# Optimization experiments

Hardware: AMD Instinct MI355X
Metric: run time of the kernel (lower is better)

Reference implementation:

```python
import jax, jax.numpy as jnp
import numpy as np

S = 32   # parent grid side
G = 64   # child grid side (2*S)
C = 16   # channels
DN = ('NDHWC', 'DHWIO', 'NDHWC')


def conv3(t, w, b):
    # t: [D,H,W,Cin] dense grid; zero padding == nonexistent coords contribute 0 (ME semantics)
    return jax.lax.conv_general_dilated(t[None], w, (1, 1, 1), 'SAME', dimension_numbers=DN)[0] + b


def _grids():
    ix = jnp.arange(G)
    px = (ix % 2)[:, None, None]
    py = (ix % 2)[None, :, None]
    pz = (ix % 2)[None, None, :]
    oct_m = {(a, b, c): (px == a) & (py == b) & (pz == c)
             for a in (0, 1) for b in (0, 1) for c in (0, 1)}
    groups6 = [[(0, 0, 0)], [(1, 1, 0)], [(1, 0, 1)], [(0, 1, 1)],
               [(1, 0, 0), (0, 1, 0)], [(0, 0, 1), (1, 1, 1)]]
    g6 = [jnp.any(jnp.stack([oct_m[o] for o in g]), 0) for g in groups6]
    s3 = (ix // 2)[:, None, None] + (ix // 2)[None, :, None] + (ix // 2)[None, None, :]
    m3 = [(s3 % 3) == j for j in range(3)]  # 3-way repartition (group_mask_gen_par)
    return g6, m3


def coder(feat, occ, w1, b1, w2, b2):
    # ProbCoder: conv -> ReLU -> conv -> sigmoid; outputs exist only at input coords
    of = occ[..., None].astype(feat.dtype)
    h = jax.nn.relu(conv3(feat, w1, b1)) * of
    return jax.nn.sigmoid(conv3(h, w2, b2)) * of


def union(a, b):
    (fa, oa), (fb, ob) = a, b
    return (jnp.where(oa[..., None], fa, fb), oa | ob)


def _forward(x, w_down, b_down, w_fel1, b_fel1, w_fel2, b_fel2, w_up, b_up,
             wc1, bc1, wc2, bc2, wl1, bl1, wl2, bl2):
    g6, m3 = _grids()
    occ_x = x[..., 0] > 0                                    # GT occupied child voxels
    # down (stride-2 conv): coordinate effect only -- last_POV uses ones_like features
    p_occ = jnp.any(occ_x.reshape(S, 2, S, 2, S, 2), axis=(1, 3, 5))  # parent coords
    pf = p_occ[..., None].astype(x.dtype)                    # last_POV features (ones)
    # FEL (dfa): conv(1->C,k3)+ReLU+conv(C->C,k3), outputs only at existing parents
    h = jax.nn.relu(conv3(pf, w_fel1, b_fel1)) * pf
    h = conv3(h, w_fel2, b_fel2) * pf                        # [S,S,S,C]
    # generative transposed conv k2 s2: each parent emits 8 children (octant-specific weight)
    up = jnp.einsum('xyzc,ocd->xyzod', h, w_up) + b_up       # [S,S,S,8,C]
    up = up.reshape(S, S, S, 2, 2, 2, C).transpose(0, 3, 1, 4, 2, 5, 6).reshape(G, G, G, C)
    occ = jnp.repeat(jnp.repeat(jnp.repeat(p_occ, 2, 0), 2, 1), 2, 2)  # child coords of prob
    prob_f = up * occ[..., None]
    lab = [occ_x & g for g in g6]                            # generate_label: GT per group
    # ---------- anchor1 compression (3 sub-stages inside octant group 1) ----------
    a1_o = occ & g6[0]
    a1_f = prob_f * a1_o[..., None]
    r = [(a1_f * m[..., None], a1_o & m) for m in m3]
    lab1 = [lab[0] & m for m in m3]
    p11 = coder(r[0][0], r[0][1], wc1[0], bc1[0], wc2[0], bc2[0])
    d1s = (prob_f * lab1[0][..., None], lab1[0])             # decoded GT of sub-stage 1
    in2 = union(r[1], d1s)
    p12 = coder(in2[0], in2[1], wl1[0], bl1[0], wl2[0], bl2[0]) * (in2[1] & m3[1])[..., None]
    d2s = (prob_f * lab1[1][..., None], lab1[1])
    in3 = union(union(d1s, d2s), r[2])
    p13 = coder(in3[0], in3[1], wl1[1], bl1[1], wl2[1], bl2[1]) * (in3[1] & m3[2])[..., None]
    # ---------- anchors 2..6 ----------
    dec = (prob_f * lab[0][..., None], lab[0])               # prob_anchor1_dec
    probs = [p11, p12, p13]
    for k in range(1, 6):
        ak_o = occ & g6[k]
        ak = (prob_f * ak_o[..., None], ak_o)
        inp = union(dec, ak)
        pk = coder(inp[0], inp[1], wc1[k], bc1[k], wc2[k], bc2[k]) * (inp[1] & g6[k])[..., None]
        probs.append(pk)
        if k < 5:
            dk = (prob_f * lab[k][..., None], lab[k])
            dec = union(dec, dk)
    probs = jnp.stack([p[..., 0] for p in probs], 0)          # [8,G,G,G]
    labels = jnp.stack([lab1[0], lab1[1], lab1[2], lab[1], lab[2], lab[3], lab[4], lab[5]], 0).astype(x.dtype)
    return probs, labels


def setup_inputs() -> dict:
    key = jax.random.key(0)
    ks = jax.random.split(key, 20)
    f = lambda k, s: jax.random.normal(k, s, jnp.float32) * 0.1
    x = (jax.random.uniform(ks[0], (G, G, G, 1)) < 0.5).astype(jnp.float32)
    return {
        'x': x,
        'w_down': f(ks[1], (2, 2, 2, 1, 1)), 'b_down': f(ks[2], (1,)),
        'w_fel1': f(ks[3], (3, 3, 3, 1, C)), 'b_fel1': f(ks[4], (C,)),
        'w_fel2': f(ks[5], (3, 3, 3, C, C)), 'b_fel2': f(ks[6], (C,)),
        'w_up': f(ks[7], (8, C, C)), 'b_up': f(ks[8], (C,)),
        'wc1': f(ks[9], (6, 3, 3, 3, C, C)), 'bc1': f(ks[10], (6, C)),
        'wc2': f(ks[11], (6, 3, 3, 3, C, 1)), 'bc2': f(ks[12], (6, 1)),
        'wl1': f(ks[13], (2, 5, 5, 5, C, C)), 'bl1': f(ks[14], (2, C)),
        'wl2': f(ks[15], (2, 5, 5, 5, C, 1)), 'bl2': f(ks[16], (2, 1)),
    }


def reference(x, w_down, b_down, w_fel1, b_fel1, w_fel2, b_fel2, w_up, b_up,
              wc1, bc1, wc2, bc2, wl1, bl1, wl2, bl2):
    return _forward(x, w_down, b_down, w_fel1, b_fel1, w_fel2, b_fel2, w_up, b_up,
                    wc1, bc1, wc2, bc2, wl1, bl1, wl2, bl2)
```

## Files before the change

kernel.cpp:

```cpp
#include <hip/hip_runtime.h>
#include <cstdint>
#include <math.h>

#define G 64
#define S 32
#define G3 (G*G*G)
#define S3 (S*S*S)

typedef unsigned long long u64;
typedef unsigned int u32;
typedef unsigned short u16;

typedef __attribute__((ext_vector_type(8))) short s16x8;
typedef __attribute__((ext_vector_type(4))) float f32x4;

__device__ __forceinline__ float sigmoidf_(float v) {
    return 1.0f / (1.0f + expf(-v));
}
__device__ __forceinline__ u32 f2bf_rne(float f) {
    u32 u = __float_as_uint(f);
    u += 0x7fff + ((u >> 16) & 1);
    return u >> 16;
}
__device__ __forceinline__ u64 rfl64(u64 v) {
    u32 lo = __builtin_amdgcn_readfirstlane((u32)v);
    u32 hi = __builtin_amdgcn_readfirstlane((u32)(v >> 32));
    return ((u64)hi << 32) | lo;
}
__device__ __forceinline__ u64 tap_hit(u64 wout, u64 wn, int dz) {
    return (dz >= 0) ? (wout & (wn >> dz)) : (wout & (wn << (-dz)));
}

__global__ __launch_bounds__(256) void k_pocc(const float* __restrict__ x,
                                              unsigned char* __restrict__ pocc) {
    int p = blockIdx.x * 256 + threadIdx.x;
    if (p >= S3) return;
    int pz = p & 31, py = (p >> 5) & 31, px = p >> 10;
    const float* b = x + (((size_t)(px * 2) * G + py * 2) * G + pz * 2);
    bool occ = false;
    #pragma unroll
    for (int a = 0; a < 2; a++)
        #pragma unroll
        for (int bb = 0; bb < 2; bb++)
            #pragma unroll
            for (int c = 0; c < 2; c++)
                occ = occ || (b[((size_t)a * G + bb) * G + c] > 0.0f);
    pocc[p] = occ ? 1 : 0;
}

__global__ __launch_bounds__(256) void k_fel1(const unsigned char* __restrict__ pocc,
                                              const float* __restrict__ w1,
                                              const float* __restrict__ b1,
                                              float* __restrict__ h1) {
    int p = blockIdx.x * 256 + threadIdx.x;
    if (p >= S3) return;
    int pz = p & 31, py = (p >> 5) & 31, px = p >> 10;
    float* o = h1 + (size_t)p * 16;
    if (!pocc[p]) {
        #pragma unroll
        for (int i = 0; i < 16; i++) o[i] = 0.0f;
        return;
    }
    float acc[16];
    #pragma unroll
    for (int i = 0; i < 16; i++) acc[i] = b1[i];
    for (int dx = -1; dx <= 1; ++dx) {
        int nx = px + dx; if ((unsigned)nx >= S) continue;
        for (int dy = -1; dy <= 1; ++dy) {
            int ny = py + dy; if ((unsigned)ny >= S) continue;
            for (int dz = -1; dz <= 1; ++dz) {
                int nz = pz + dz; if ((unsigned)nz >= S) continue;
                if (pocc[(nx * S + ny) * S + nz]) {
                    const float* w = w1 + (((dx + 1) * 3 + (dy + 1)) * 3 + (dz + 1)) * 16;
                    #pragma unroll
                    for (int i = 0; i < 16; i++) acc[i] += w[i];
                }
            }
        }
    }
    #pragma unroll
    for (int i = 0; i < 16; i++) o[i] = fmaxf(acc[i], 0.0f);
}

__global__ __launch_bounds__(256) void k_fel2(const unsigned char* __restrict__ pocc,
                                              const float* __restrict__ h1,
                                              const float* __restrict__ w2,
                                              const float* __restrict__ b2,
                                              float* __restrict__ h2) {
    int p = blockIdx.x * 256 + threadIdx.x;
    if (p >= S3) return;
    int pz = p & 31, py = (p >> 5) & 31, px = p >> 10;
    float* o = h2 + (size_t)p * 16;
    if (!pocc[p]) {
        #pragma unroll
        for (int i = 0; i < 16; i++) o[i] = 0.0f;
        return;
    }
    float acc[16];
    #pragma unroll
    for (int i = 0; i < 16; i++) acc[i] = b2[i];
    for (int dx = -1; dx <= 1; ++dx) {
        int nx = px + dx; if ((unsigned)nx >= S) continue;
        for (int dy = -1; dy <= 1; ++dy) {
            int ny = py + dy; if ((unsigned)ny >= S) continue;
            for (int dz = -1; dz <= 1; ++dz) {
                int nz = pz + dz; if ((unsigned)nz >= S) continue;
                const float* f = h1 + (size_t)((nx * S + ny) * S + nz) * 16;
                const float* w = w2 + (((dx + 1) * 3 + (dy + 1)) * 3 + (dz + 1)) * 256;
                #pragma unroll
                for (int ci = 0; ci < 16; ++ci) {
                    float fv = f[ci];
                    #pragma unroll
                    for (int co = 0; co < 16; ++co)
                        acc[co] = fmaf(fv, w[ci * 16 + co], acc[co]);
                }
            }
        }
    }
    #pragma unroll
    for (int i = 0; i < 16; i++) o[i] = acc[i];
}

__global__ __launch_bounds__(256) void k_up(const unsigned char* __restrict__ pocc,
                                            const float* __restrict__ h2,
                                            const float* __restrict__ wup,
                                            const float* __restrict__ bup,
                                            u16* __restrict__ pf) {
    int p = blockIdx.x * 256 + threadIdx.x;
    if (p >= S3) return;
    int pz = p & 31, py = (p >> 5) & 31, px = p >> 10;
    bool occ = pocc[p] != 0;
    float h[16];
    const float* hp = h2 + (size_t)p * 16;
    #pragma unroll
    for (int i = 0; i < 16; i++) h[i] = hp[i];
    #pragma unroll
    for (int o = 0; o < 8; o++) {
        int a = o >> 2, b = (o >> 1) & 1, c = o & 1;
        u16* op = pf + (((size_t)(2 * px + a) * G + (2 * py + b)) * G + (2 * pz + c)) * 16;
        uint4* o4 = reinterpret_cast<uint4*>(op);
        if (!occ) {
            o4[0] = make_uint4(0, 0, 0, 0);
            o4[1] = make_uint4(0, 0, 0, 0);
        } else {
            u32 pk[8];
            #pragma unroll
            for (int i = 0; i < 8; ++i) {
                float a0 = bup[2 * i], a1 = bup[2 * i + 1];
                #pragma unroll
                for (int cc = 0; cc < 16; cc++) {
                    a0 = fmaf(h[cc], wup[(o * 16 + cc) * 16 + 2 * i], a0);
                    a1 = fmaf(h[cc], wup[(o * 16 + cc) * 16 + 2 * i + 1], a1);
                }
                pk[i] = f2bf_rne(a0) | (f2bf_rne(a1) << 16);
            }
            o4[0] = make_uint4(pk[0], pk[1], pk[2], pk[3]);
            o4[1] = make_uint4(pk[4], pk[5], pk[6], pk[7]);
        }
    }
}

__global__ __launch_bounds__(256) void k_masks(const float* __restrict__ x,
                                               const unsigned char* __restrict__ pocc,
                                               u64* __restrict__ lw_in,
                                               u64* __restrict__ lw_fin,
                                               float* __restrict__ labels) {
    int z = threadIdx.x;
    int y = blockIdx.x * 4 + threadIdx.y;
    int xx = blockIdx.y;
    int v = (xx * G + y) * G + z;
    int par = ((xx & 1) << 2) | ((y & 1) << 1) | (z & 1);
    const int gmap[8] = {0, 5, 4, 3, 4, 2, 1, 5};
    int g = gmap[par];
    int t = ((xx >> 1) + (y >> 1) + (z >> 1)) % 3;
    bool occ = pocc[(((xx >> 1) * S) + (y >> 1)) * S + (z >> 1)] != 0;
    bool ox = x[v] > 0.0f;
    bool g0 = (g == 0);

    bool mi[8], mf[8], lb[8];
    mi[0] = occ && g0 && (t == 0);
    mi[1] = (occ && g0 && (t == 1)) || (ox && g0 && (t == 0));
    mi[2] = (ox && g0 && (t < 2)) || (occ && g0 && (t == 2));
    mi[3] = (ox && g0)       || (occ && (g == 1));
    mi[4] = (ox && (g <= 1)) || (occ && (g == 2));
    mi[5] = (ox && (g <= 2)) || (occ && (g == 3));
    mi[6] = (ox && (g <= 3)) || (occ && (g == 4));
    mi[7] = (ox && (g <= 4)) || (occ && (g == 5));

    mf[0] = occ && g0 && (t == 0);
    mf[1] = occ && g0 && (t == 1);
    mf[2] = occ && g0 && (t == 2);
    mf[3] = occ && (g == 1);
    mf[4] = occ && (g == 2);
    mf[5] = occ && (g == 3);
    mf[6] = occ && (g == 4);
    mf[7] = occ && (g == 5);

    lb[0] = ox && g0 && (t == 0);
    lb[1] = ox && g0 && (t == 1);
    lb[2] = ox && g0 && (t == 2);
    lb[3] = ox && (g == 1);
    lb[4] = ox && (g == 2);
    lb[5] = ox && (g == 3);
    lb[6] = ox && (g == 4);
    lb[7] = ox && (g == 5);

    int line = xx * G + y;
    #pragma unroll
    for (int c = 0; c < 8; ++c) {
        u64 wi = __ballot((int)mi[c]);
        u64 wf = __ballot((int)mf[c]);
        if (z == 0) {
            lw_in[c * 4096 + line] = wi;
            lw_fin[c * 4096 + line] = wf;
        }
        labels[(size_t)c * G3 + v] = lb[c] ? 1.0f : 0.0f;
    }
}

#define FRAGSTRIDE 38400
__global__ __launch_bounds__(64) void k_prep_bfrag(const float* __restrict__ wc1,
                                                   const float* __restrict__ wl1,
                                                   u16* __restrict__ bfrag) {
    int c = blockIdx.x;
    int frag = blockIdx.y;
    int lane = threadIdx.x;
    bool is5 = (c == 1 || c == 2);
    int R = is5 ? 2 : 1;
    int KS = 2 * R + 1;
    int npair = R + 1;
    int nfrag = KS * KS * npair;
    if (frag >= nfrag) return;
    const float* W = is5 ? (wl1 + (size_t)(c - 1) * 32000)
                         : (wc1 + (size_t)((c == 0) ? 0 : (c - 2)) * 6912);
    int dxdy = frag / npair, p = frag - dxdy * npair;
    int dziA = 2 * p;
    int co = lane & 15, kg = lane >> 4;
    u16 outv[8];
    #pragma unroll
    for (int j = 0; j < 8; ++j) {
        int k = kg * 8 + j;
        int ci = k & 15;
        int dzi = (k < 16) ? dziA : (dziA + 1);
        float v = 0.0f;
        if (dzi < KS)
            v = W[(size_t)(dxdy * KS + dzi) * 256 + ci * 16 + co];
        outv[j] = (u16)f2bf_rne(v);
    }
    u16* o = bfrag + (size_t)c * FRAGSTRIDE + ((size_t)frag * 64 + lane) * 8;
    uint4 pk;
    pk.x = outv[0] | ((u32)outv[1] << 16);
    pk.y = outv[2] | ((u32)outv[3] << 16);
    pk.z = outv[4] | ((u32)outv[5] << 16);
    pk.w = outv[6] | ((u32)outv[7] << 16);
    *reinterpret_cast<uint4*>(o) = pk;
}

__global__ __launch_bounds__(256) void k_conv1_mfma(const u16* __restrict__ pf,
                                                    const u64* __restrict__ lw_in,
                                                    const u16* __restrict__ bfrag,
                                                    const float* __restrict__ bc1,
                                                    const float* __restrict__ bl1,
                                                    u16* __restrict__ hbase) {
    int c = blockIdx.y;
    bool is5 = (c == 1 || c == 2);
    int R = is5 ? 2 : 1;
    int KS = 2 * R + 1, npair = R + 1;
    const u64* lw = lw_in + (size_t)c * 4096;
    u16* h_c = hbase + (size_t)c * G3 * 16;
    const u16* bf = bfrag + (size_t)c * FRAGSTRIDE;
    const float* bptr = is5 ? (bl1 + (c - 1) * 16)
                            : (bc1 + ((c == 0) ? 0 : (c - 2)) * 16);

    int x = blockIdx.x >> 4;
    int y0 = (blockIdx.x & 15) << 2;
    int w = threadIdx.y;
    int lane = threadIdx.x;
    int yw = y0 + w;

    u64 w0 = rfl64(lw[x * G + yw]);
    u64 anyw = lw[x * G + y0] | lw[x * G + y0 + 1] | lw[x * G + y0 + 2] | lw[x * G + y0 + 3];
    if (anyw == 0ULL) return;

    __shared__ u32 lds[8 * 2304 / 4];

    int col = lane & 15, kg = lane >> 4;
    float bv = bptr[col];
    f32x4 acc[4];
    #pragma unroll
    for (int s = 0; s < 4; ++s) acc[s] = (f32x4){bv, bv, bv, bv};

    int nlines = 4 + 2 * R;
    int nunits = nlines * 144;
    int t = w * 64 + lane;

    for (int dx = -R; dx <= R; ++dx) {
        int nx = x + dx;
        __syncthreads();
        if ((unsigned)nx < G) {
            for (int u = t; u < nunits; u += 256) {
                int s = u / 144; int q = u - s * 144;
                int lz = q >> 1, half = q & 1;
                int gz = lz - 4;
                int ny = y0 - R + s;
                uint4 val = make_uint4(0, 0, 0, 0);
                if ((unsigned)ny < G && (unsigned)gz < G) {
                    u64 wn = lw[nx * G + ny];
                    if ((wn >> gz) & 1)
                        val = *reinterpret_cast<const uint4*>(
                            pf + ((size_t)((nx * G + ny) * G + gz) * 16 + half * 8));
                }
                *reinterpret_cast<uint4*>(
                    reinterpret_cast<char*>(lds) + s * 2304 + lz * 32 +
                    ((half ^ ((lz >> 2) & 1)) * 16)) = val;
            }
        }
        __syncthreads();
        if (w0 == 0ULL || (unsigned)nx >= G) continue;

        for (int dy = -R; dy <= R; ++dy) {
            int ny = yw + dy;
            if ((unsigned)ny >= G) continue;
            u64 wn = rfl64(lw[nx * G + ny]);
            if (wn == 0ULL) continue;
            int slot = w + dy + R;
            for (int p = 0; p < npair; ++p) {
                int dzA = -R + 2 * p;
                int dzB = dzA + 1;
                bool hasB = (dzB <= R);
                u64 hit = tap_hit(w0, wn, dzA);
                if (hasB) hit |= tap_hit(w0, wn, dzB);
                if (hit == 0ULL) continue;
                int frag = ((dx + R) * KS + (dy + R)) * npair + p;
                s16x8 bf8 = *reinterpret_cast<const s16x8*>(bf + ((size_t)frag * 64 + lane) * 8);
                int dz = (kg < 2) ? dzA : (hasB ? dzB : dzA);
                int lzb = col + dz + 4;
                const char* ab = reinterpret_cast<const char*>(lds)
                                 + slot * 2304 + lzb * 32
                                 + (((kg & 1) ^ ((lzb >> 2) & 1)) * 16);
                #pragma unroll
                for (int s = 0; s < 4; ++s) {
                    if (((hit >> (s * 16)) & 0xFFFFULL) == 0ULL) continue;
                    s16x8 a = *reinterpret_cast<const s16x8*>(ab + s * 512);
                    acc[s] = __builtin_amdgcn_mfma_f32_16x16x32_bf16(a, bf8, acc[s], 0, 0, 0);
                }
            }
        }
    }

    if (w0 == 0ULL) return;
    u16* hline = h_c + (size_t)(x * G + yw) * G * 16;
    #pragma unroll
    for (int s = 0; s < 4; ++s) {
        #pragma unroll
        for (int r = 0; r < 4; ++r) {
            int z = s * 16 + kg * 4 + r;
            if ((w0 >> z) & 1) {
                float v = fmaxf(acc[s][r], 0.0f);
                hline[z * 16 + col] = (u16)f2bf_rne(v);
            }
        }
    }
}

template <int KS>
__device__ __forceinline__ void conv2_body(const u32* __restrict__ h_c,
                                           const u64* __restrict__ lwi,
                                           const u64* __restrict__ lwf,
                                           const float* __restrict__ w2,
                                           const float* __restrict__ b2,
                                           float* __restrict__ outp) {
    const int R = KS / 2;
    int z = threadIdx.x;
    int line = blockIdx.x * 4 + threadIdx.y;
    int xx = line >> 6, y = line & 63;
    int v = (xx * G + y) * G + z;
    u64 wf = rfl64(lwf[line]);
    if (wf == 0ULL) { outp[v] = 0.0f; return; }
    bool m = (wf >> z) & 1;

    float ac0 = 0.0f, ac1 = 0.0f;
    for (int dx = -R; dx <= R; ++dx) {
        int nx = xx + dx; if ((unsigned)nx >= G) continue;
        for (int dy = -R; dy <= R; ++dy) {
            int ny = y + dy; if ((unsigned)ny >= G) continue;
            u64 wn = rfl64(lwi[nx * G + ny]);
            if (wn == 0ULL) continue;
            const float* wbase = w2 + (size_t)(((dx + R) * KS + (dy + R)) * KS) * 16;
            #pragma unroll
            for (int dz = -R; dz <= R; ++dz) {
                if (tap_hit(wf, wn, dz) == 0ULL) continue;
                int nz = z + dz;
                bool ok = (unsigned)nz < G;
                int nzc = ok ? nz : 0;
                bool mn = ok && ((wn >> nzc) & 1);
                const float* w = wbase + (dz + R) * 16;
                if (mn) {
                    const uint4* h4 = reinterpret_cast<const uint4*>(
                        h_c + ((size_t)((nx * G + ny) * G + nzc)) * 8);
                    uint4 Ua = h4[0], Ub = h4[1];
                    u32 uu[8] = {Ua.x, Ua.y, Ua.z, Ua.w, Ub.x, Ub.y, Ub.z, Ub.w};
                    float s0 = 0.0f, s1 = 0.0f;
                    #pragma unroll
                    for (int i = 0; i < 8; ++i) {
                        float lo = __uint_as_float(uu[i] << 16);
                        float hi = __uint_as_float(uu[i] & 0xffff0000u);
                        s0 = fmaf(lo, w[2 * i], s0);
                        s1 = fmaf(hi, w[2 * i + 1], s1);
                    }
                    if (((dz + R) & 1) == 0) ac0 += s0 + s1;
                    else                     ac1 += s0 + s1;
                }
            }
        }
    }
    float acc = b2[0] + ac0 + ac1;
    outp[v] = m ? sigmoidf_(acc) : 0.0f;
}

__global__ __launch_bounds__(256) void k_conv2_all(const u32* __restrict__ hbase,
                                                   const u64* __restrict__ lw_in,
                                                   const u64* __restrict__ lw_fin,
                                                   const float* __restrict__ wc2,
                                                   const float* __restrict__ bc2,
                                                   const float* __restrict__ wl2,
                                                   const float* __restrict__ bl2,
                                                   float* __restrict__ out) {
    int c = blockIdx.y;
    const u64* lwi = lw_in + (size_t)c * 4096;
    const u64* lwf = lw_fin + (size_t)c * 4096;
    const u32* h_c = hbase + (size_t)c * G3 * 8;
    float* outp = out + (size_t)c * G3;
    if (c == 1 || c == 2) {
        conv2_body<5>(h_c, lwi, lwf, wl2 + (size_t)(c - 1) * 2000, bl2 + (c - 1), outp);
    } else {
        int j = (c == 0) ? 0 : (c - 2);
        conv2_body<3>(h_c, lwi, lwf, wc2 + (size_t)j * 432, bc2 + j, outp);
    }
}

extern "C" void kernel_launch(void* const* d_in, const int* in_sizes, int n_in,
                              void* d_out, int out_size, void* d_ws, size_t ws_size,
                              hipStream_t stream) {
    const float* x      = (const float*)d_in[0];
    const float* w_fel1 = (const float*)d_in[3];
    const float* b_fel1 = (const float*)d_in[4];
    const float* w_fel2 = (const float*)d_in[5];
    const float* b_fel2 = (const float*)d_in[6];
    const float* w_up   = (const float*)d_in[7];
    const float* b_up   = (const float*)d_in[8];
    const float* wc1    = (const float*)d_in[9];
    const float* bc1    = (const float*)d_in[10];
    const float* wc2    = (const float*)d_in[11];
    const float* bc2    = (const float*)d_in[12];
    const float* wl1    = (const float*)d_in[13];
    const float* bl1    = (const float*)d_in[14];
    const float* wl2    = (const float*)d_in[15];
    const float* bl2    = (const float*)d_in[16];
    float* out = (float*)d_out;

    char* ws = (char*)d_ws;
    u16*  probf16 = (u16*)(ws);
    float* h1     = (float*)(ws + 8388608);
    float* h2     = (float*)(ws + 10485760);
    unsigned char* pocc = (unsigned char*)(ws + 12582912);
    u64* lw_in  = (u64*)(ws + 12615680);
    u64* lw_fin = (u64*)(ws + 12877824);
    u16* bfrag  = (u16*)(ws + 13139968);
    u16* hbase  = (u16*)(ws + 13754368);

    k_pocc <<<dim3(S3 / 256), dim3(256), 0, stream>>>(x, pocc);
    k_fel1 <<<dim3(S3 / 256), dim3(256), 0, stream>>>(pocc, w_fel1, b_fel1, h1);
    k_fel2 <<<dim3(S3 / 256), dim3(256), 0, stream>>>(pocc, h1, w_fel2, b_fel2, h2);
    k_up   <<<dim3(S3 / 256), dim3(256), 0, stream>>>(pocc, h2, w_up, b_up, probf16);
    k_masks<<<dim3(16, 64), dim3(64, 4), 0, stream>>>(x, pocc, lw_in, lw_fin, out + (size_t)8 * G3);
    k_prep_bfrag<<<dim3(8, 75), dim3(64), 0, stream>>>(wc1, wl1, bfrag);

    k_conv1_mfma<<<dim3(1024, 8), dim3(64, 4), 0, stream>>>(
        probf16, lw_in, bfrag, bc1, bl1, hbase);
    k_conv2_all<<<dim3(1024, 8), dim3(64, 4), 0, stream>>>(
        (const u32*)hbase, lw_in, lw_fin, wc2, bc2, wl2, bl2, out);
}
```

Baseline: 213.3 us.

## Pre-mask conv1 inputs per coder and stage them into LDS with direct global loads

The FEL and upsample kernels now give each thread one output channel (or one octant) instead of a whole voxel, which multiplies thread count and shrinks per-thread work. A new pass materializes per-coder masked bf16 probability grids, so conv1 can stream full lines into LDS with global_load_lds instead of per-voxel masked, bit-tested loads. Coders are processed in batches sized to the workspace. In exchange this writes and reads up to 8 extra 8 MB buffers and adds launches, and it depends on LDS zero-padding and the swizzle matching the direct-load layout.

```diff
diff --git a/kernel.cpp b/kernel.cpp
--- a/kernel.cpp
+++ b/kernel.cpp
@@ -29,6 +29,11 @@
 }
 __device__ __forceinline__ u64 tap_hit(u64 wout, u64 wn, int dz) {
     return (dz >= 0) ? (wout & (wn >> dz)) : (wout & (wn << (-dz)));
+}
+__device__ __forceinline__ void gload16(const void* g, void* l) {
+    __builtin_amdgcn_global_load_lds(
+        (const __attribute__((address_space(1))) unsigned int*)g,
+        (__attribute__((address_space(3))) unsigned int*)l, 16, 0, 0);
 }
 
 __global__ __launch_bounds__(256) void k_pocc(const float* __restrict__ x,
@@ -52,34 +57,23 @@
                                               const float* __restrict__ w1,
                                               const float* __restrict__ b1,
                                               float* __restrict__ h1) {
-    int p = blockIdx.x * 256 + threadIdx.x;
-    if (p >= S3) return;
+    int idx = blockIdx.x * 256 + threadIdx.x;
+    int p = idx >> 4, co = idx & 15;
     int pz = p & 31, py = (p >> 5) & 31, px = p >> 10;
-    float* o = h1 + (size_t)p * 16;
-    if (!pocc[p]) {
-        #pragma unroll
-        for (int i = 0; i < 16; i++) o[i] = 0.0f;
-        return;
-    }
-    float acc[16];
-    #pragma unroll
-    for (int i = 0; i < 16; i++) acc[i] = b1[i];
+    if (!pocc[p]) { h1[idx] = 0.0f; return; }
+    float a = b1[co];
     for (int dx = -1; dx <= 1; ++dx) {
         int nx = px + dx; if ((unsigned)nx >= S) continue;
         for (int dy = -1; dy <= 1; ++dy) {
             int ny = py + dy; if ((unsigned)ny >= S) continue;
             for (int dz = -1; dz <= 1; ++dz) {
                 int nz = pz + dz; if ((unsigned)nz >= S) continue;
-                if (pocc[(nx * S + ny) * S + nz]) {
-                    const float* w = w1 + (((dx + 1) * 3 + (dy + 1)) * 3 + (dz + 1)) * 16;
-                    #pragma unroll
-                    for (int i = 0; i < 16; i++) acc[i] += w[i];
-                }
-            }
-        }
-    }
-    #pragma unroll
-    for (int i = 0; i < 16; i++) o[i] = fmaxf(acc[i], 0.0f);
+                if (pocc[(nx * S + ny) * S + nz])
+                    a += w1[(((dx + 1) * 3 + (dy + 1)) * 3 + (dz + 1)) * 16 + co];
+            }
+        }
+    }
+    h1[idx] = fmaxf(a, 0.0f);
 }
 
 __global__ __launch_bounds__(256) void k_fel2(const unsigned char* __restrict__ pocc,
@@ -87,18 +81,11 @@
                                               const float* __restrict__ w2,
                                               const float* __restrict__ b2,
                                               float* __restrict__ h2) {
-    int p = blockIdx.x * 256 + threadIdx.x;
-    if (p >= S3) return;
+    int idx = blockIdx.x * 256 + threadIdx.x;
+    int p = idx >> 4, co = idx & 15;
     int pz = p & 31, py = (p >> 5) & 31, px = p >> 10;
-    float* o = h2 + (size_t)p * 16;
-    if (!pocc[p]) {
-        #pragma unroll
-        for (int i = 0; i < 16; i++) o[i] = 0.0f;
-        return;
-    }
-    float acc[16];
-    #pragma unroll
-    for (int i = 0; i < 16; i++) acc[i] = b2[i];
+    if (!pocc[p]) { h2[idx] = 0.0f; return; }
+    float a = b2[co];
     for (int dx = -1; dx <= 1; ++dx) {
         int nx = px + dx; if ((unsigned)nx >= S) continue;
         for (int dy = -1; dy <= 1; ++dy) {
@@ -106,19 +93,14 @@
             for (int dz = -1; dz <= 1; ++dz) {
                 int nz = pz + dz; if ((unsigned)nz >= S) continue;
                 const float* f = h1 + (size_t)((nx * S + ny) * S + nz) * 16;
-                const float* w = w2 + (((dx + 1) * 3 + (dy + 1)) * 3 + (dz + 1)) * 256;
+                const float* ww = w2 + (size_t)(((dx + 1) * 3 + (dy + 1)) * 3 + (dz + 1)) * 256 + co;
                 #pragma unroll
-                for (int ci = 0; ci < 16; ++ci) {
-                    float fv = f[ci];
-                    #pragma unroll
-                    for (int co = 0; co < 16; ++co)
-                        acc[co] = fmaf(fv, w[ci * 16 + co], acc[co]);
-                }
-            }
-        }
-    }
-    #pragma unroll
-    for (int i = 0; i < 16; i++) o[i] = acc[i];
+                for (int ci = 0; ci < 16; ++ci)
+                    a = fmaf(f[ci], ww[ci * 16], a);
+            }
+        }
+    }
+    h2[idx] = a;
 }
 
 __global__ __launch_bounds__(256) void k_up(const unsigned char* __restrict__ pocc,
@@ -126,44 +108,43 @@
                                             const float* __restrict__ wup,
                                             const float* __restrict__ bup,
                                             u16* __restrict__ pf) {
-    int p = blockIdx.x * 256 + threadIdx.x;
-    if (p >= S3) return;
+    int idx = blockIdx.x * 256 + threadIdx.x;
+    int p = idx >> 3, o = idx & 7;
     int pz = p & 31, py = (p >> 5) & 31, px = p >> 10;
     bool occ = pocc[p] != 0;
+    int a = o >> 2, b = (o >> 1) & 1, c = o & 1;
+    int line = (2 * px + a) * G + (2 * py + b);
+    u16* op = pf + ((size_t)line * 64 + (2 * pz + c)) * 16;
+    uint4* o4 = reinterpret_cast<uint4*>(op);
+    if (!occ) {
+        o4[0] = make_uint4(0, 0, 0, 0);
+        o4[1] = make_uint4(0, 0, 0, 0);
+        return;
+    }
     float h[16];
     const float* hp = h2 + (size_t)p * 16;
     #pragma unroll
     for (int i = 0; i < 16; i++) h[i] = hp[i];
-    #pragma unroll
-    for (int o = 0; o < 8; o++) {
-        int a = o >> 2, b = (o >> 1) & 1, c = o & 1;
-        u16* op = pf + (((size_t)(2 * px + a) * G + (2 * py + b)) * G + (2 * pz + c)) * 16;
-        uint4* o4 = reinterpret_cast<uint4*>(op);
-        if (!occ) {
-            o4[0] = make_uint4(0, 0, 0, 0);
-            o4[1] = make_uint4(0, 0, 0, 0);
-        } else {
-            u32 pk[8];
-            #pragma unroll
-            for (int i = 0; i < 8; ++i) {
-                float a0 = bup[2 * i], a1 = bup[2 * i + 1];
-                #pragma unroll
-                for (int cc = 0; cc < 16; cc++) {
-                    a0 = fmaf(h[cc], wup[(o * 16 + cc) * 16 + 2 * i], a0);
-                    a1 = fmaf(h[cc], wup[(o * 16 + cc) * 16 + 2 * i + 1], a1);
-                }
-                pk[i] = f2bf_rne(a0) | (f2bf_rne(a1) << 16);
-            }
-            o4[0] = make_uint4(pk[0], pk[1], pk[2], pk[3]);
-            o4[1] = make_uint4(pk[4], pk[5], pk[6], pk[7]);
-        }
-    }
+    u32 pk[8];
+    #pragma unroll
+    for (int i = 0; i < 8; ++i) {
+        float a0 = bup[2 * i], a1 = bup[2 * i + 1];
+        #pragma unroll
+        for (int cc = 0; cc < 16; cc++) {
+            a0 = fmaf(h[cc], wup[(o * 16 + cc) * 16 + 2 * i], a0);
+            a1 = fmaf(h[cc], wup[(o * 16 + cc) * 16 + 2 * i + 1], a1);
+        }
+        pk[i] = f2bf_rne(a0) | (f2bf_rne(a1) << 16);
+    }
+    o4[0] = make_uint4(pk[0], pk[1], pk[2], pk[3]);
+    o4[1] = make_uint4(pk[4], pk[5], pk[6], pk[7]);
 }
 
 __global__ __launch_bounds__(256) void k_masks(const float* __restrict__ x,
                                                const unsigned char* __restrict__ pocc,
                                                u64* __restrict__ lw_in,
                                                u64* __restrict__ lw_fin,
+                                               unsigned char* __restrict__ m_in,
                                                float* __restrict__ labels) {
     int z = threadIdx.x;
     int y = blockIdx.x * 4 + threadIdx.y;
@@ -206,6 +187,7 @@
     lb[7] = ox && (g == 5);
 
     int line = xx * G + y;
+    u32 mbyte = 0;
     #pragma unroll
     for (int c = 0; c < 8; ++c) {
         u64 wi = __ballot((int)mi[c]);
@@ -214,7 +196,25 @@
             lw_in[c * 4096 + line] = wi;
             lw_fin[c * 4096 + line] = wf;
         }
+        mbyte |= ((u32)mi[c]) << c;
         labels[(size_t)c * G3 + v] = lb[c] ? 1.0f : 0.0f;
+    }
+    m_in[v] = (unsigned char)mbyte;
+}
+
+__global__ __launch_bounds__(256) void k_maskprob(const u16* __restrict__ pf,
+                                                  const unsigned char* __restrict__ m_in,
+                                                  u16* __restrict__ mprob,
+                                                  int b0, int nb) {
+    int gid = blockIdx.x * 256 + threadIdx.x;
+    size_t off = (size_t)gid * 8;
+    uint4 d = *reinterpret_cast<const uint4*>(pf + off);
+    unsigned char mb = m_in[gid >> 1];
+    const uint4 z = make_uint4(0, 0, 0, 0);
+    for (int ci = 0; ci < nb; ++ci) {
+        int c = b0 + ci;
+        uint4 o = ((mb >> c) & 1) ? d : z;
+        *reinterpret_cast<uint4*>(mprob + (size_t)ci * G3 * 16 + off) = o;
     }
 }
 
@@ -256,18 +256,21 @@
     *reinterpret_cast<uint4*>(o) = pk;
 }
 
-__global__ __launch_bounds__(256) void k_conv1_mfma(const u16* __restrict__ pf,
+__global__ __launch_bounds__(256) void k_conv1_mfma(const u16* __restrict__ mprob,
                                                     const u64* __restrict__ lw_in,
                                                     const u16* __restrict__ bfrag,
                                                     const float* __restrict__ bc1,
                                                     const float* __restrict__ bl1,
-                                                    u16* __restrict__ hbase) {
-    int c = blockIdx.y;
+                                                    u16* __restrict__ hbase,
+                                                    int b0) {
+    int ci = blockIdx.y;
+    int c = b0 + ci;
     bool is5 = (c == 1 || c == 2);
     int R = is5 ? 2 : 1;
     int KS = 2 * R + 1, npair = R + 1;
     const u64* lw = lw_in + (size_t)c * 4096;
-    u16* h_c = hbase + (size_t)c * G3 * 16;
+    u16* h_c = hbase + (size_t)ci * G3 * 16;
+    const u16* mp = mprob + (size_t)ci * G3 * 16;
     const u16* bf = bfrag + (size_t)c * FRAGSTRIDE;
     const float* bptr = is5 ? (bl1 + (c - 1) * 16)
                             : (bc1 + ((c == 0) ? 0 : (c - 2)) * 16);
@@ -283,6 +286,7 @@
     if (anyw == 0ULL) return;
 
     __shared__ u32 lds[8 * 2304 / 4];
+    char* ldsc = reinterpret_cast<char*>(lds);
 
     int col = lane & 15, kg = lane >> 4;
     float bv = bptr[col];
@@ -290,29 +294,30 @@
     #pragma unroll
     for (int s = 0; s < 4; ++s) acc[s] = (f32x4){bv, bv, bv, bv};
 
+    int t = w * 64 + lane;
+    if (t < 128) {
+        int slot = t >> 4, q = t & 15;
+        int off = (q < 8) ? (q * 16) : (2176 + (q - 8) * 16);
+        *reinterpret_cast<uint4*>(ldsc + slot * 2304 + off) = make_uint4(0, 0, 0, 0);
+    }
+
+    u32 goff = ((u32)lane >> 1) * 32 +
+               ((((u32)lane & 1) ^ (((u32)lane >> 3) & 1) ^ 1u) * 16);
+
     int nlines = 4 + 2 * R;
-    int nunits = nlines * 144;
-    int t = w * 64 + lane;
 
     for (int dx = -R; dx <= R; ++dx) {
         int nx = x + dx;
         __syncthreads();
         if ((unsigned)nx < G) {
-            for (int u = t; u < nunits; u += 256) {
-                int s = u / 144; int q = u - s * 144;
-                int lz = q >> 1, half = q & 1;
-                int gz = lz - 4;
+            for (int s = w; s < nlines; s += 4) {
                 int ny = y0 - R + s;
-                uint4 val = make_uint4(0, 0, 0, 0);
-                if ((unsigned)ny < G && (unsigned)gz < G) {
-                    u64 wn = lw[nx * G + ny];
-                    if ((wn >> gz) & 1)
-                        val = *reinterpret_cast<const uint4*>(
-                            pf + ((size_t)((nx * G + ny) * G + gz) * 16 + half * 8));
-                }
-                *reinterpret_cast<uint4*>(
-                    reinterpret_cast<char*>(lds) + s * 2304 + lz * 32 +
-                    ((half ^ ((lz >> 2) & 1)) * 16)) = val;
+                if ((unsigned)ny >= G) continue;
+                if (lw[nx * G + ny] == 0ULL) continue;
+                const char* src = reinterpret_cast<const char*>(mp + (size_t)(nx * G + ny) * 1024) + goff;
+                char* dst = ldsc + s * 2304 + 128;
+                gload16(src, dst);
+                gload16(src + 1024, dst + 1024);
             }
         }
         __syncthreads();
@@ -335,8 +340,7 @@
                 s16x8 bf8 = *reinterpret_cast<const s16x8*>(bf + ((size_t)frag * 64 + lane) * 8);
                 int dz = (kg < 2) ? dzA : (hasB ? dzB : dzA);
                 int lzb = col + dz + 4;
-                const char* ab = reinterpret_cast<const char*>(lds)
-                                 + slot * 2304 + lzb * 32
+                const char* ab = ldsc + slot * 2304 + lzb * 32
                                  + (((kg & 1) ^ ((lzb >> 2) & 1)) * 16);
                 #pragma unroll
                 for (int s = 0; s < 4; ++s) {
@@ -425,11 +429,13 @@
                                                    const float* __restrict__ bc2,
                                                    const float* __restrict__ wl2,
                                                    const float* __restrict__ bl2,
-                                                   float* __restrict__ out) {
-    int c = blockIdx.y;
+                                                   float* __restrict__ out,
+                                                   int b0) {
+    int ci = blockIdx.y;
+    int c = b0 + ci;
     const u64* lwi = lw_in + (size_t)c * 4096;
     const u64* lwf = lw_fin + (size_t)c * 4096;
-    const u32* h_c = hbase + (size_t)c * G3 * 8;
+    const u32* h_c = hbase + (size_t)ci * G3 * 8;
     float* outp = out + (size_t)c * G3;
     if (c == 1 || c == 2) {
         conv2_body<5>(h_c, lwi, lwf, wl2 + (size_t)(c - 1) * 2000, bl2 + (c - 1), outp);
@@ -467,17 +473,27 @@
     u64* lw_in  = (u64*)(ws + 12615680);
     u64* lw_fin = (u64*)(ws + 12877824);
     u16* bfrag  = (u16*)(ws + 13139968);
-    u16* hbase  = (u16*)(ws + 13754368);
+    unsigned char* m_in = (unsigned char*)(ws + 8388608);
+    u16* mprob  = (u16*)(ws + 13754368);
+
+    int NB = 4;
+    if (13754368 + (size_t)16 * 8388608 <= ws_size) NB = 8;
+    u16* hbase = (u16*)(ws + 13754368 + (size_t)NB * 8388608);
 
     k_pocc <<<dim3(S3 / 256), dim3(256), 0, stream>>>(x, pocc);
-    k_fel1 <<<dim3(S3 / 256), dim3(256), 0, stream>>>(pocc, w_fel1, b_fel1, h1);
-    k_fel2 <<<dim3(S3 / 256), dim3(256), 0, stream>>>(pocc, h1, w_fel2, b_fel2, h2);
-    k_up   <<<dim3(S3 / 256), dim3(256), 0, stream>>>(pocc, h2, w_up, b_up, probf16);
-    k_masks<<<dim3(16, 64), dim3(64, 4), 0, stream>>>(x, pocc, lw_in, lw_fin, out + (size_t)8 * G3);
+    k_fel1 <<<dim3(S3 * 16 / 256), dim3(256), 0, stream>>>(pocc, w_fel1, b_fel1, h1);
+    k_fel2 <<<dim3(S3 * 16 / 256), dim3(256), 0, stream>>>(pocc, h1, w_fel2, b_fel2, h2);
+    k_up   <<<dim3(S3 * 8 / 256), dim3(256), 0, stream>>>(pocc, h2, w_up, b_up, probf16);
+    k_masks<<<dim3(16, 64), dim3(64, 4), 0, stream>>>(x, pocc, lw_in, lw_fin, m_in,
+                                                      out + (size_t)8 * G3);
     k_prep_bfrag<<<dim3(8, 75), dim3(64), 0, stream>>>(wc1, wl1, bfrag);
 
-    k_conv1_mfma<<<dim3(1024, 8), dim3(64, 4), 0, stream>>>(
-        probf16, lw_in, bfrag, bc1, bl1, hbase);
-    k_conv2_all<<<dim3(1024, 8), dim3(64, 4), 0, stream>>>(
-        (const u32*)hbase, lw_in, lw_fin, wc2, bc2, wl2, bl2, out);
-}
+    for (int b0 = 0; b0 < 8; b0 += NB) {
+        int nb = (8 - b0 < NB) ? (8 - b0) : NB;
+        k_maskprob<<<dim3(G3 * 16 / 8 / 256), dim3(256), 0, stream>>>(probf16, m_in, mprob, b0, nb);
+        k_conv1_mfma<<<dim3(1024, nb), dim3(64, 4), 0, stream>>>(
+            mprob, lw_in, bfrag, bc1, bl1, hbase, b0);
+        k_conv2_all<<<dim3(1024, nb), dim3(64, 4), 0, stream>>>(
+            (const u32*)hbase, lw_in, lw_fin, wc2, bc2, wl2, bl2, out, b0);
+    }
+}
```

Result: no change. 210.9 us (-1.1%).
